# Kernel tuning notes

Hardware: AMD Instinct MI355X
Metric: run time of the kernel (lower is better)

Reference implementation:

```python
import jax, jax.numpy as jnp
import numpy as np

B, H, W, C = 4, 48, 48, 768
L = H * W
D_STATE, D_CONV, D_INNER = 16, 4, C  # expand=1
DT_RANK = (C + 15) // 16  # 48


def generate_cross_scan_indices(Hh, Ww):
    indices = []
    visited = set()
    ch, cw = Hh // 2, Ww // 2
    indices.append((ch, cw)); visited.add((ch, cw))
    for radius in range(1, max(Hh, Ww)):
        for r in range(1, radius + 1):
            p = (ch - r, cw)
            if 0 <= p[0] < Hh and 0 <= p[1] < Ww and p not in visited: indices.append(p); visited.add(p)
        for r in range(1, radius + 1):
            p = (ch, cw + r)
            if 0 <= p[0] < Hh and 0 <= p[1] < Ww and p not in visited: indices.append(p); visited.add(p)
        for r in range(1, radius + 1):
            p = (ch + r, cw)
            if 0 <= p[0] < Hh and 0 <= p[1] < Ww and p not in visited: indices.append(p); visited.add(p)
        for r in range(1, radius + 1):
            p = (ch, cw - r)
            if 0 <= p[0] < Hh and 0 <= p[1] < Ww and p not in visited: indices.append(p); visited.add(p)
        for r in range(1, radius + 1):
            for p in [(ch - r, cw + r), (ch + r, cw + r), (ch + r, cw - r), (ch - r, cw - r)]:
                if 0 <= p[0] < Hh and 0 <= p[1] < Ww and p not in visited: indices.append(p); visited.add(p)
        for i in range(-radius, radius + 1):
            for j in range(-radius, radius + 1):
                p = (ch + i, cw + j)
                if 0 <= p[0] < Hh and 0 <= p[1] < Ww and p not in visited: indices.append(p); visited.add(p)
    return np.array([i * Ww + j for i, j in indices], dtype=np.int32)


def _mamba_params(key, scale=0.02):
    ks = jax.random.split(key, 6)
    return dict(
        in_w=jax.random.normal(ks[0], (2 * D_INNER, C)) * scale,
        conv_w=jax.random.normal(ks[1], (D_INNER, 1, D_CONV)) * scale,
        conv_b=jnp.zeros((D_INNER,)),
        xproj_w=jax.random.normal(ks[2], (DT_RANK + 2 * D_STATE, D_INNER)) * scale,
        dt_w=jax.random.normal(ks[3], (D_INNER, DT_RANK)) * scale,
        dt_b=jax.random.normal(ks[4], (D_INNER,)) * 0.1,
        A_log=jnp.broadcast_to(jnp.log(jnp.arange(1, D_STATE + 1, dtype=jnp.float32)), (D_INNER, D_STATE)).copy(),
        Dp=jnp.ones((D_INNER,)),
        out_w=jax.random.normal(ks[5], (C, D_INNER)) * scale,
    )


def setup_inputs() -> dict:
    key = jax.random.key(0)
    kx, kf, kb, k1, k2 = jax.random.split(key, 5)
    fp = _mamba_params(kf)
    bp = _mamba_params(kb)
    inp = {
        'x': jax.random.normal(kx, (B, L, C), dtype=jnp.float32),
        'scan_idx': jnp.asarray(generate_cross_scan_indices(H, W)),
        'norm_g': jnp.ones((C,)), 'norm_b': jnp.zeros((C,)),
        'fuse_w1': jax.random.normal(k1, (C, 2 * C)) * 0.02, 'fuse_b1': jnp.zeros((C,)),
        'fuse_w2': jax.random.normal(k2, (C, C)) * 0.02, 'fuse_b2': jnp.zeros((C,)),
    }
    for pre, p in (('f_', fp), ('b_', bp)):
        for n, v in p.items():
            inp[pre + n] = v
    return inp


def silu(v):
    return v * jax.nn.sigmoid(v)


def mamba(x, in_w, conv_w, conv_b, xproj_w, dt_w, dt_b, A_log, Dp, out_w):
    Bn, Ln, _ = x.shape
    xz = x @ in_w.T                      # [B,L,2*d_inner]
    xi, z = jnp.split(xz, 2, axis=-1)
    # causal depthwise conv1d, kernel D_CONV, left pad D_CONV-1
    xp = jnp.pad(xi, ((0, 0), (D_CONV - 1, 0), (0, 0)))
    xc = sum(conv_w[:, 0, k] * xp[:, k:k + Ln, :] for k in range(D_CONV)) + conv_b
    xc = silu(xc)                        # [B,L,d_inner]
    x_dbl = xc @ xproj_w.T
    dt, Bm, Cm = jnp.split(x_dbl, [DT_RANK, DT_RANK + D_STATE], axis=-1)
    dt = jax.nn.softplus(dt @ dt_w.T + dt_b)  # [B,L,d_inner]
    A = -jnp.exp(A_log)                  # [d_inner,d_state]

    def step(h, inps):
        dt_t, B_t, C_t, x_t = inps       # [B,d],[B,s],[B,s],[B,d]
        dA = jnp.exp(dt_t[:, :, None] * A)
        h = dA * h + (dt_t * x_t)[:, :, None] * B_t[:, None, :]
        y = jnp.einsum('bds,bs->bd', h, C_t)
        return h, y

    h0 = jnp.zeros((Bn, D_INNER, D_STATE), xc.dtype)
    xs = (dt.transpose(1, 0, 2), Bm.transpose(1, 0, 2), Cm.transpose(1, 0, 2), xc.transpose(1, 0, 2))
    _, ys = jax.lax.scan(step, h0, xs)
    y = ys.transpose(1, 0, 2) + Dp * xc
    y = y * silu(z)
    return y @ out_w.T


def reference(x, scan_idx, norm_g, norm_b, fuse_w1, fuse_b1, fuse_w2, fuse_b2,
              f_in_w, f_conv_w, f_conv_b, f_xproj_w, f_dt_w, f_dt_b, f_A_log, f_Dp, f_out_w,
              b_in_w, b_conv_w, b_conv_b, b_xproj_w, b_dt_w, b_dt_b, b_A_log, b_Dp, b_out_w):
    residual = x
    mu = x.mean(-1, keepdims=True)
    var = ((x - mu) ** 2).mean(-1, keepdims=True)
    xn = (x - mu) / jnp.sqrt(var + 1e-6) * norm_g + norm_b
    rev = jnp.argsort(scan_idx)
    xf = mamba(xn[:, scan_idx, :], f_in_w, f_conv_w, f_conv_b, f_xproj_w, f_dt_w, f_dt_b, f_A_log, f_Dp, f_out_w)[:, rev, :]
    flip = scan_idx[::-1]
    xb = mamba(xn[:, flip, :], b_in_w, b_conv_w, b_conv_b, b_xproj_w, b_dt_w, b_dt_b, b_A_log, b_Dp, b_out_w)[:, jnp.argsort(flip), :]
    fused = jnp.concatenate([xf, xb], axis=-1)
    h = jax.nn.gelu(fused @ fuse_w1.T + fuse_b1, approximate=False)
    out = h @ fuse_w2.T + fuse_b2
    return out + residual
```

## Files before the change

kernel.cpp:

```cpp
#include <hip/hip_runtime.h>
#include <hip/hip_bf16.h>
#include <cmath>

#define BB 4
#define LL 2304
#define CC 768
#define DSTATE 16
#define DINNER 768
#define DTRANK 48
#define MTOK (BB*LL)
#define NCH 48
#define LCH (LL/NCH)

#define S_XZ   14155776L
#define S_XC   7077888L
#define S_DT   7077888L
#define S_BC   294912L
#define S_YB   7077888L
#define S_AP   2359296L

typedef __bf16 bf16_t;
typedef __bf16 bf16x8 __attribute__((ext_vector_type(8)));
typedef float  f32x4  __attribute__((ext_vector_type(4)));

__device__ __forceinline__ float silu_f(float v){ return v / (1.0f + __expf(-v)); }
__device__ __forceinline__ float softplus_f(float v){
    return fmaxf(v,0.f) + __logf(1.0f + __expf(-fabsf(v)));
}

typedef __attribute__((address_space(3))) void  lds_vt;
typedef __attribute__((address_space(1))) void  gbl_vt;
__device__ __forceinline__ void async_copy16(const void* g, void* l){
    __builtin_amdgcn_global_load_lds((const gbl_vt*)g, (lds_vt*)l, 16, 0, 0);
}

__global__ __launch_bounds__(256)
void wconv_k(const float* __restrict__ a0, const float* __restrict__ a1,
             const float* __restrict__ a2, const float* __restrict__ a3,
             const float* __restrict__ a4, const float* __restrict__ a5,
             bf16_t* __restrict__ dst)
{
    const int cum[7]  = {0,1179648,2359296,3538944,4128768,4153344,4177920};
    const int dofs[6] = {0,1179648,2359296,3538944,4718592,5332992};
    const float* srcs[6] = {a0,a1,a2,a3,a4,a5};
    int idx = blockIdx.x*256 + threadIdx.x;
    if (idx >= 4177920) return;
    int seg = 0;
    while (idx >= cum[seg+1]) ++seg;
    dst[dofs[seg] + idx - cum[seg]] = (bf16_t)srcs[seg][idx - cum[seg]];
}

__global__ __launch_bounds__(256)
void transp_k(const float* __restrict__ s0, const float* __restrict__ s1,
              bf16_t* __restrict__ d0, bf16_t* __restrict__ d1)
{
    __shared__ float tile[32][33];
    const float* src = blockIdx.z ? s1 : s0;
    bf16_t* dst = blockIdx.z ? d1 : d0;
    int c0 = blockIdx.y*32, d0c = blockIdx.x*32;
    int tx = threadIdx.x & 31, ty = threadIdx.x >> 5;
#pragma unroll
    for (int r=0;r<4;++r)
        tile[ty+8*r][tx] = src[(long)(c0+ty+8*r)*768 + d0c+tx];
    __syncthreads();
#pragma unroll
    for (int r=0;r<4;++r)
        dst[(long)(d0c+ty+8*r)*768 + c0+tx] = (bf16_t)tile[tx][ty+8*r];
}

__global__ __launch_bounds__(256)
void inv_k(const int* __restrict__ sidx, int* __restrict__ rf, int* __restrict__ rb)
{
    int t = blockIdx.x*256 + threadIdx.x;
    if (t >= LL) return;
    rf[sidx[t]] = t;
    rb[sidx[LL-1-t]] = t;
}

__global__ __launch_bounds__(256)
void combo_k(const float* __restrict__ dtw, const float* __restrict__ xproj,
             bf16_t* __restrict__ dst)
{
    __shared__ float row[48];
    int n = blockIdx.x;
    if (threadIdx.x < 48) row[threadIdx.x] = dtw[n*48 + threadIdx.x];
    __syncthreads();
#pragma unroll
    for (int kk=0; kk<3; ++kk){
        int k = threadIdx.x + 256*kk;
        float s = 0.f;
#pragma unroll 8
        for (int r=0; r<48; ++r) s += row[r]*xproj[r*768 + k];
        dst[n*768 + k] = (bf16_t)s;
    }
}

__global__ __launch_bounds__(256)
void ln_k(const float* __restrict__ x, const float* __restrict__ g,
          const float* __restrict__ bta, bf16_t* __restrict__ xn)
{
    int row = blockIdx.x;
    const float* xr = x + (long)row*CC;
    int tid = threadIdx.x;
    float v[3];
#pragma unroll
    for (int r=0;r<3;++r) v[r] = xr[tid + 256*r];
    float s  = v[0]+v[1]+v[2];
    float s2 = v[0]*v[0]+v[1]*v[1]+v[2]*v[2];
    __shared__ float red[8];
    for (int o=32;o;o>>=1){ s += __shfl_down(s,o); s2 += __shfl_down(s2,o); }
    int wv = tid>>6, ln = tid&63;
    if (ln==0){ red[wv]=s; red[4+wv]=s2; }
    __syncthreads();
    if (tid==0){
        red[0] = red[0]+red[1]+red[2]+red[3];
        red[4] = red[4]+red[5]+red[6]+red[7];
    }
    __syncthreads();
    float mu  = red[0]*(1.0f/CC);
    float var = red[4]*(1.0f/CC) - mu*mu;
    float rstd = rsqrtf(var + 1e-6f);
#pragma unroll
    for (int r=0;r<3;++r){
        int c = tid + 256*r;
        xn[(long)row*CC + c] = (bf16_t)((v[r]-mu)*rstd*g[c] + bta[c]);
    }
}

#define CT 8
__global__ __launch_bounds__(256)
void conv_k(const bf16_t* __restrict__ xz, const float* __restrict__ cw0,
            const float* __restrict__ cw1, const float* __restrict__ cb0,
            const float* __restrict__ cb1, bf16_t* __restrict__ xc)
{
    int dir = blockIdx.y;
    const bf16_t* xzd = xz + (long)dir*S_XZ;
    const float* cw = dir ? cw1 : cw0;
    const float* cb = dir ? cb1 : cb0;
    bf16_t* xcd = xc + (long)dir*S_XC;
    int idx = blockIdx.x*256 + threadIdx.x;
    if (idx >= (MTOK/CT)*(DINNER/8)) return;
    int dg    = idx % (DINNER/8);
    int chunk = idx / (DINNER/8);
    int d0 = dg*8;
    long r0 = (long)chunk*CT;
    int t0 = (int)(r0 % LL);

    float4 wv[8];
#pragma unroll
    for (int u=0;u<8;++u) wv[u] = *(const float4*)&cw[(d0+u)*4];
    float bz[8];
#pragma unroll
    for (int u=0;u<8;++u) bz[u] = cb[d0+u];

    const bf16_t* src = xzd + r0*1536 + d0;
    bf16x8 win0, win1, win2;
    if (t0 >= 3){
        win0 = *(const bf16x8*)(src - 3*1536);
        win1 = *(const bf16x8*)(src - 2*1536);
        win2 = *(const bf16x8*)(src - 1*1536);
    } else {
#pragma unroll
        for (int u=0;u<8;++u){ win0[u]=(bf16_t)0.f; win1[u]=(bf16_t)0.f; win2[u]=(bf16_t)0.f; }
    }
#pragma unroll
    for (int t=0;t<CT;++t){
        bf16x8 cur = *(const bf16x8*)(src + (long)t*1536);
        bf16x8 o;
#pragma unroll
        for (int u=0;u<8;++u){
            float acc = bz[u]
                + wv[u].x*(float)win0[u] + wv[u].y*(float)win1[u]
                + wv[u].z*(float)win2[u] + wv[u].w*(float)cur[u];
            o[u] = (bf16_t)silu_f(acc);
        }
        *(bf16x8*)(xcd + (r0+t)*DINNER + d0) = o;
        win0 = win1; win1 = win2; win2 = cur;
    }
}

template<int GATHER, int SCATTER, int EPI>
__global__ __launch_bounds__(256)
void gemm4_k(const bf16_t* __restrict__ A, long a_stride, int lda,
             const bf16_t* __restrict__ W0, const bf16_t* __restrict__ W1,
             int N, int K,
             void* __restrict__ out1, long o1_stride,
             void* __restrict__ out2, long o2_stride,
             int ldc, int ccol_stride,
             const float* __restrict__ bias0, const float* __restrict__ bias1,
             const float* __restrict__ resid,
             const int* __restrict__ sidx,
             const int* __restrict__ ridx0, const int* __restrict__ ridx1)
{
    __shared__ __align__(16) bf16_t smem[2*128*64];
    bf16_t* As = smem;
    bf16_t* Bs = smem + 128*64;

    const int tid  = threadIdx.x;
    const int lane = tid & 63;
    const int w    = tid >> 6;
    const int ln16 = lane & 15;
    const int q    = lane >> 4;
    const int dir  = blockIdx.z;

    const bf16_t* Ad = A + (long)dir*a_stride;
    const bf16_t* W  = dir ? W1 : W0;
    const float* bias = dir ? bias1 : bias0;

    const int m0 = blockIdx.x*128;
    const int n0 = blockIdx.y*128;

    const int srow = lane >> 3;
    const int csrc = (lane & 7) ^ srow;
    const bf16_t* gA[4]; const bf16_t* gA1[4]; const bf16_t* gB[4];
#pragma unroll
    for (int inst=0; inst<4; ++inst){
        int row = w*32 + inst*8 + srow;
        int r = m0 + row;
        if (GATHER == 4){
            int t = r % LL; int bo = r - t;
            gA[inst]  = A + (long)(bo + ridx0[t])*lda + csrc*8;
            gA1[inst] = A + a_stride + (long)(bo + ridx1[t])*lda + csrc*8;
        } else {
            int sr = r;
            if (GATHER == 3){
                int t = r % LL; int bo = r - t;
                sr = bo + (dir ? sidx[LL-1-t] : sidx[t]);
            }
            gA[inst] = Ad + (long)sr*lda + csrc*8;
        }
        int n = n0 + row; if (n >= N) n = N-1;
        gB[inst] = W + (long)n*K + csrc*8;
    }

    f32x4 acc[4][4];
#pragma unroll
    for (int i=0;i<4;++i)
#pragma unroll
      for (int j=0;j<4;++j) acc[i][j] = (f32x4){0.f,0.f,0.f,0.f};

    const int e = ln16 & 7;
    const int ar_base = ((w>>1)*64 + ln16)*64;
    const int br_base = ((w&1)*64 + ln16)*64;

    for (int k0 = 0; k0 < K; k0 += 64){
#pragma unroll
        for (int inst=0; inst<4; ++inst){
            bf16_t* la = As + (w*256 + inst*64)*8;
            bf16_t* lb = Bs + (w*256 + inst*64)*8;
            const bf16_t* asrc;
            if (GATHER == 4)
                asrc = (k0 >= 768) ? (gA1[inst] + (k0 - 768)) : (gA[inst] + k0);
            else
                asrc = gA[inst] + k0;
            async_copy16(asrc, la);
            async_copy16(gB[inst] + k0, lb);
        }
        __syncthreads();
#pragma unroll
        for (int kk=0; kk<2; ++kk){
            const int ce = (((kk<<2)|q) ^ e)*8;
            bf16x8 af[4], bf[4];
#pragma unroll
            for (int i=0;i<4;++i) af[i] = *(const bf16x8*)&As[ar_base + i*16*64 + ce];
#pragma unroll
            for (int j=0;j<4;++j) bf[j] = *(const bf16x8*)&Bs[br_base + j*16*64 + ce];
#pragma unroll
            for (int i=0;i<4;++i)
#pragma unroll
              for (int j=0;j<4;++j)
                acc[i][j] = __builtin_amdgcn_mfma_f32_16x16x32_bf16(af[i], bf[j], acc[i][j], 0,0,0);
        }
        __syncthreads();
    }

    const int mw = (w>>1)*64;
    const int nw = (w&1)*64;
    const int ccolb = ccol_stride*dir;

    const bool staged = (EPI==2) || (EPI==3) || (EPI==5 && n0 < 768);
    if (staged){
        bf16_t* Cs = smem;
#pragma unroll
        for (int i=0;i<4;++i){
#pragma unroll
            for (int reg=0; reg<4; ++reg){
                int rowl = mw + i*16 + q*4 + reg;
#pragma unroll
                for (int j=0;j<4;++j){
                    int coll = nw + j*16 + ln16;
                    float v = acc[i][j][reg];
                    if (EPI==3){
                        v += bias[n0 + coll];
                        v = 0.5f*v*(1.0f + erff(v*0.70710678118654752f));
                    } else if (EPI==5){
                        v = softplus_f(v + bias[n0 + coll]);
                    }
                    Cs[rowl*128 + coll] = (bf16_t)v;
                }
            }
        }
        __syncthreads();
        bf16_t* o = (bf16_t*)out1 + (long)dir*o1_stride;
#pragma unroll
        for (int c=0;c<8;++c){
            int chunk = tid + 256*c;
            int rowl = chunk >> 4;
            int coll = (chunk & 15)*8;
            int r = m0 + rowl;
            int orow = r;
            if (SCATTER == 3){
                int t = r % LL; int bo = r - t;
                orow = bo + (dir ? sidx[LL-1-t] : sidx[t]);
            }
            *(int4*)&o[(long)orow*ldc + ccolb + n0 + coll] = *(const int4*)&Cs[rowl*128 + coll];
        }
    } else {
#pragma unroll
        for (int i=0;i<4;++i){
#pragma unroll
            for (int reg=0; reg<4; ++reg){
                int r = m0 + mw + i*16 + q*4 + reg;
#pragma unroll
                for (int j=0;j<4;++j){
                    int col = n0 + nw + j*16 + ln16;
                    if (col >= N) continue;
                    float v = acc[i][j][reg];
                    if (EPI==4){
                        v += bias[col] + resid[(long)r*CC + col];
                        ((float*)out1)[(long)r*ldc + col] = v;
                    } else {
                        ((float*)out2 + (long)dir*o2_stride)[(long)r*32 + (col-768)] = v;
                    }
                }
            }
        }
    }
}

template<int PASS>
__global__ __launch_bounds__(256)
void scanp_k(const bf16_t* __restrict__ dtp, const bf16_t* __restrict__ xcp,
             const float* __restrict__ bcp, const bf16_t* __restrict__ xzp,
             const float* __restrict__ Al0, const float* __restrict__ Al1,
             const float* __restrict__ Dp0, const float* __restrict__ Dp1,
             float* __restrict__ Aprod, float* __restrict__ Hend,
             bf16_t* __restrict__ yout)
{
    extern __shared__ __align__(16) char smem[];
    bf16_t* s_dt = (bf16_t*)smem;
    bf16_t* s_xc = (bf16_t*)(smem + 6144);
    float*  s_bc = (float*) (smem + 12288);
    bf16_t* s_z  = (bf16_t*)(smem + 18432);
    bf16_t* s_y  = (bf16_t*)(smem + 24576);

    int dir = blockIdx.y;
    int blk = blockIdx.x;
    int dblk = blk % 12; int tmp = blk / 12;
    int j = tmp % NCH; int b = tmp / NCH;
    int tid = threadIdx.x;
    long tbase = (long)b*LL + (long)j*LCH;

    const bf16_t* gdt = dtp + dir*S_DT + tbase*DINNER + dblk*64;
    const bf16_t* gxc = xcp + dir*S_XC + tbase*DINNER + dblk*64;
    const float*  gbc = bcp + dir*S_BC + tbase*32;
    {
        int c = tid, t = c>>3, dc = c&7;
        async_copy16(gdt + (long)t*DINNER + dc*8, s_dt + c*8);
        async_copy16(gxc + (long)t*DINNER + dc*8, s_xc + c*8);
        async_copy16(gbc + (long)t*32 + dc*4, s_bc + c*4);
        if (tid < 128){
            c = tid + 256; t = c>>3; dc = c&7;
            async_copy16(gdt + (long)t*DINNER + dc*8, s_dt + c*8);
            async_copy16(gxc + (long)t*DINNER + dc*8, s_xc + c*8);
            async_copy16(gbc + (long)t*32 + dc*4, s_bc + c*4);
        }
    }
    if (PASS==3){
        const bf16_t* gz = xzp + dir*S_XZ + tbase*1536 + DINNER + dblk*64;
        int c = tid, t = c>>3, dc = c&7;
        async_copy16(gz + (long)t*1536 + dc*8, s_z + c*8);
        if (tid < 128){ c = tid+256; t = c>>3; dc = c&7;
            async_copy16(gz + (long)t*1536 + dc*8, s_z + c*8); }
    }
    __syncthreads();

    int lane = tid & 63, w = tid >> 6;
    int d_low = lane & 15, sg = lane >> 4;
    int dl = w*16 + d_low;
    int d  = dblk*64 + dl;

    const float* Al = dir ? Al1 : Al0;
    f32x4 al = *(const f32x4*)&Al[d*DSTATE + sg*4];
    float a_c[4];
#pragma unroll
    for (int k=0;k<4;++k) a_c[k] = -__expf(al[k]);

    float h[4] = {0.f,0.f,0.f,0.f};
    float dpv = 0.f;
    long o = dir*S_AP + ((long)(b*NCH + j)*DINNER + d)*DSTATE + sg*4;
    if (PASS==3){
        f32x4 hin = *(const f32x4*)&Aprod[o];
#pragma unroll
        for (int k=0;k<4;++k) h[k] = hin[k];
        dpv = (dir ? Dp1 : Dp0)[d];
    }
    float sdt = 0.f;

    for (int t=0; t<LCH; ++t){
        float dt = (float)s_dt[t*64 + dl];
        float xv = (float)s_xc[t*64 + dl];
        f32x4 Bv = *(const f32x4*)&s_bc[t*32 + sg*4];
        float c = dt*xv;
        if (PASS==1) sdt += dt;
#pragma unroll
        for (int k=0;k<4;++k){
            float da = __expf(dt * a_c[k]);
            h[k] = da*h[k] + c*Bv[k];
        }
        if (PASS==3){
            f32x4 Cv = *(const f32x4*)&s_bc[t*32 + 16 + sg*4];
            float p = h[0]*Cv[0] + h[1]*Cv[1] + h[2]*Cv[2] + h[3]*Cv[3];
            p += __shfl_xor(p, 16);
            p += __shfl_xor(p, 32);
            if (sg == 0){
                float z = (float)s_z[t*64 + dl];
                s_y[t*64 + dl] = (bf16_t)((p + dpv*xv) * silu_f(z));
            }
        }
    }

    if (PASS==1){
        f32x4 ap, hv;
#pragma unroll
        for (int k=0;k<4;++k){ ap[k] = __expf(sdt * a_c[k]); hv[k] = h[k]; }
        *(f32x4*)&Aprod[o] = ap;
        *(f32x4*)&Hend[o]  = hv;
    }
    if (PASS==3){
        __syncthreads();
        bf16_t* gy = yout + dir*S_YB + tbase*DINNER + dblk*64;
        int c = tid, t = c>>3, dc = c&7;
        *(int4*)(gy + (long)t*DINNER + dc*8) = *(const int4*)&s_y[c*8];
        if (tid < 128){ c = tid+256; t = c>>3; dc = c&7;
            *(int4*)(gy + (long)t*DINNER + dc*8) = *(const int4*)&s_y[c*8]; }
    }
}

__global__ __launch_bounds__(256)
void scan2_k(float* __restrict__ Aprod, const float* __restrict__ Hend)
{
    int idx = blockIdx.x*256 + threadIdx.x;
    if (idx >= 2*BB*DINNER*DSTATE) return;
    int dir = idx / (BB*DINNER*DSTATE);
    int rem = idx - dir*(BB*DINNER*DSTATE);
    int b = rem / (DINNER*DSTATE);
    int ds = rem % (DINNER*DSTATE);
    long base = (long)dir*S_AP;
    float h = 0.f;
    for (int j=0;j<NCH;++j){
        long o = base + (long)(b*NCH+j)*DINNER*DSTATE + ds;
        float ap = Aprod[o];
        float he = Hend[o];
        Aprod[o] = h;
        h = ap*h + he;
    }
}

extern "C" void kernel_launch(void* const* d_in, const int* in_sizes, int n_in,
                              void* d_out, int out_size, void* d_ws, size_t ws_size,
                              hipStream_t stream)
{
    const float* x       = (const float*)d_in[0];
    const int*   sidx    = (const int*)  d_in[1];
    const float* norm_g  = (const float*)d_in[2];
    const float* norm_b  = (const float*)d_in[3];
    const float* fuse_w1 = (const float*)d_in[4];
    const float* fuse_b1 = (const float*)d_in[5];
    const float* fuse_w2 = (const float*)d_in[6];
    const float* fuse_b2 = (const float*)d_in[7];
    const float* f_in_w   = (const float*)d_in[8];
    const float* f_conv_w = (const float*)d_in[9];
    const float* f_conv_b = (const float*)d_in[10];
    const float* f_xproj  = (const float*)d_in[11];
    const float* f_dt_w   = (const float*)d_in[12];
    const float* f_dt_b   = (const float*)d_in[13];
    const float* f_A_log  = (const float*)d_in[14];
    const float* f_Dp     = (const float*)d_in[15];
    const float* f_out_w  = (const float*)d_in[16];
    const float* b_in_w   = (const float*)d_in[17];
    const float* b_conv_w = (const float*)d_in[18];
    const float* b_conv_b = (const float*)d_in[19];
    const float* b_xproj  = (const float*)d_in[20];
    const float* b_dt_w   = (const float*)d_in[21];
    const float* b_dt_b   = (const float*)d_in[22];
    const float* b_A_log  = (const float*)d_in[23];
    const float* b_Dp     = (const float*)d_in[24];
    const float* b_out_w  = (const float*)d_in[25];
    float* out = (float*)d_out;

    float* ws    = (float*)d_ws;
    bf16_t* xn   = (bf16_t*)ws;
    bf16_t* xz   = (bf16_t*)(ws + 3538944);
    bf16_t* xc   = (bf16_t*)(ws + 17694720);
    bf16_t* dtb  = (bf16_t*)(ws + 24772608);
    float* bc    = ws + 31850496;
    bf16_t* yb   = (bf16_t*)(ws + 32440320);
    bf16_t* h1   = (bf16_t*)(ws + 39518208);
    float* Aprod = ws + 43057152;
    float* Hend  = ws + 47775744;
    bf16_t* wbf  = (bf16_t*)(ws + 52494336);
    int* rev_f   = (int*)(ws + 56352768);
    int* rev_b   = rev_f + 2304;

    bf16_t* w_fin    = wbf + 0;
    bf16_t* w_bin    = wbf + 1179648;
    bf16_t* w_1      = wbf + 2359296;
    bf16_t* w_2      = wbf + 3538944;
    bf16_t* w_fcombo = wbf + 4128768;
    bf16_t* w_bcombo = wbf + 4743168;
    bf16_t* foutT    = wbf + 5357568;
    bf16_t* boutT    = wbf + 5947392;
    bf16_t* Ccat     = wbf + 6537216;

    wconv_k<<<16320, 256, 0, stream>>>(f_in_w, b_in_w, fuse_w1, fuse_w2,
                                       f_xproj + 48*768, b_xproj + 48*768, wbf);
    transp_k<<<dim3(24,24,2), 256, 0, stream>>>(f_out_w, b_out_w, foutT, boutT);
    inv_k<<<9, 256, 0, stream>>>(sidx, rev_f, rev_b);
    combo_k<<<768, 256, 0, stream>>>(f_dt_w, f_xproj, w_fcombo);
    combo_k<<<768, 256, 0, stream>>>(b_dt_w, b_xproj, w_bcombo);
    ln_k<<<MTOK, 256, 0, stream>>>(x, norm_g, norm_b, xn);
    gemm4_k<0,0,2><<<dim3(6,6,2), 256, 0, stream>>>(
        w_1, 768, 1536, foutT, boutT, 768, 768,
        Ccat, 0, nullptr, 0, 1536, 768, nullptr, nullptr, nullptr, nullptr,
        nullptr, nullptr);

    const unsigned lds1 = 18432, lds3 = 30720;

    gemm4_k<3,0,2><<<dim3(72,12,2), 256, 0, stream>>>(
        xn, 0, CC, w_fin, w_bin, 1536, 768,
        xz, S_XZ, nullptr, 0, 1536, 0, nullptr, nullptr, nullptr, sidx,
        nullptr, nullptr);
    conv_k<<<dim3((MTOK/CT)*(DINNER/8)/256, 2), 256, 0, stream>>>(
        xz, f_conv_w, b_conv_w, f_conv_b, b_conv_b, xc);
    gemm4_k<0,0,5><<<dim3(72,7,2), 256, 0, stream>>>(
        xc, S_XC, DINNER, w_fcombo, w_bcombo, 800, 768,
        dtb, S_DT, bc, S_BC, 768, 0, f_dt_b, b_dt_b, nullptr, nullptr,
        nullptr, nullptr);
    scanp_k<1><<<dim3(BB*NCH*12,2), 256, lds1, stream>>>(
        dtb, xc, bc, nullptr, f_A_log, b_A_log, f_Dp, b_Dp, Aprod, Hend, nullptr);
    scan2_k<<<384, 256, 0, stream>>>(Aprod, Hend);
    scanp_k<3><<<dim3(BB*NCH*12,2), 256, lds3, stream>>>(
        dtb, xc, bc, xz, f_A_log, b_A_log, f_Dp, b_Dp, Aprod, Hend, yb);
    gemm4_k<4,0,3><<<dim3(72,6,1), 256, 0, stream>>>(
        yb, S_YB, DINNER, Ccat, Ccat, 768, 1536,
        h1, 0, nullptr, 0, 768, 0, fuse_b1, fuse_b1, nullptr, nullptr,
        rev_f, rev_b);
    gemm4_k<0,0,4><<<dim3(72,6,1), 256, 0, stream>>>(
        h1, 0, DINNER, w_2, w_2, 768, 768,
        out, 0, nullptr, 0, 768, 0, fuse_b2, fuse_b2, x, nullptr,
        nullptr, nullptr);
}
```

Before: 522.2 us.

## Restructure chunked scan to one channel per thread with exp-power recurrence

The chunked selective-scan kernels now give each thread one channel and all 16 states, replacing the old 4-state split and its cross-lane shuffle reductions. dt, x and z are read straight from global memory, with only B/C staged in LDS, and each block covers 256 channels, so the grid shrinks fourfold. When A_log matches log(1..16), a runtime-checked fast path computes exp(-k*dt) as powers of a single exp2, which removes 15 of 16 transcendentals per step. The cost is more registers per thread, lower occupancy, uncoalesced-looking strided global loads for dt/x/z, and a fast path that only pays off for the standard A initialisation.

```diff
diff --git a/kernel.cpp b/kernel.cpp
--- a/kernel.cpp
+++ b/kernel.cpp
@@ -18,6 +18,8 @@
 #define S_BC   294912L
 #define S_YB   7077888L
 #define S_AP   2359296L
+
+#define L2E 1.4426950408889634f
 
 typedef __bf16 bf16_t;
 typedef __bf16 bf16x8 __attribute__((ext_vector_type(8)));
@@ -347,103 +349,115 @@
              float* __restrict__ Aprod, float* __restrict__ Hend,
              bf16_t* __restrict__ yout)
 {
-    extern __shared__ __align__(16) char smem[];
-    bf16_t* s_dt = (bf16_t*)smem;
-    bf16_t* s_xc = (bf16_t*)(smem + 6144);
-    float*  s_bc = (float*) (smem + 12288);
-    bf16_t* s_z  = (bf16_t*)(smem + 18432);
-    bf16_t* s_y  = (bf16_t*)(smem + 24576);
-
-    int dir = blockIdx.y;
+    __shared__ __align__(16) float s_bc[LCH*32];
+
+    const int dir = blockIdx.y;
     int blk = blockIdx.x;
-    int dblk = blk % 12; int tmp = blk / 12;
-    int j = tmp % NCH; int b = tmp / NCH;
-    int tid = threadIdx.x;
-    long tbase = (long)b*LL + (long)j*LCH;
-
-    const bf16_t* gdt = dtp + dir*S_DT + tbase*DINNER + dblk*64;
-    const bf16_t* gxc = xcp + dir*S_XC + tbase*DINNER + dblk*64;
-    const float*  gbc = bcp + dir*S_BC + tbase*32;
-    {
-        int c = tid, t = c>>3, dc = c&7;
-        async_copy16(gdt + (long)t*DINNER + dc*8, s_dt + c*8);
-        async_copy16(gxc + (long)t*DINNER + dc*8, s_xc + c*8);
-        async_copy16(gbc + (long)t*32 + dc*4, s_bc + c*4);
-        if (tid < 128){
-            c = tid + 256; t = c>>3; dc = c&7;
-            async_copy16(gdt + (long)t*DINNER + dc*8, s_dt + c*8);
-            async_copy16(gxc + (long)t*DINNER + dc*8, s_xc + c*8);
-            async_copy16(gbc + (long)t*32 + dc*4, s_bc + c*4);
-        }
-    }
+    const int dblk = blk % 3; int tmp = blk / 3;
+    const int j = tmp % NCH; const int b = tmp / NCH;
+    const int tid = threadIdx.x;
+    const long tbase = (long)b*LL + (long)j*LCH;
+    const int d = dblk*256 + tid;
+
+    const float* gbc = bcp + dir*S_BC + tbase*32;
+    async_copy16(gbc + tid*4, s_bc + tid*4);
+    if (tid < 128) async_copy16(gbc + (256+tid)*4, s_bc + (256+tid)*4);
+
+    const float* Al = dir ? Al1 : Al0;
+    float ac2[16]; bool fast = true;
+#pragma unroll
+    for (int k=0;k<16;++k){
+        float a = -__expf(Al[d*DSTATE + k]);
+        fast = fast && (fabsf(a + (float)(k+1)) < 1e-3f*(float)(k+1));
+        ac2[k] = a * L2E;
+    }
+
+    __syncthreads();
+
+    const bf16_t* gdt = dtp + dir*S_DT + tbase*DINNER + d;
+    const bf16_t* gxc = xcp + dir*S_XC + tbase*DINNER + d;
+    const bf16_t* gz  = xzp + dir*S_XZ + tbase*1536 + DINNER + d;
+    bf16_t* gy = yout + dir*S_YB + tbase*DINNER + d;
+
+    const long o = dir*S_AP + ((long)(b*NCH + j)*DINNER + d)*DSTATE;
+
+    float h[16];
+    float dpv = 0.f;
     if (PASS==3){
-        const bf16_t* gz = xzp + dir*S_XZ + tbase*1536 + DINNER + dblk*64;
-        int c = tid, t = c>>3, dc = c&7;
-        async_copy16(gz + (long)t*1536 + dc*8, s_z + c*8);
-        if (tid < 128){ c = tid+256; t = c>>3; dc = c&7;
-            async_copy16(gz + (long)t*1536 + dc*8, s_z + c*8); }
-    }
-    __syncthreads();
-
-    int lane = tid & 63, w = tid >> 6;
-    int d_low = lane & 15, sg = lane >> 4;
-    int dl = w*16 + d_low;
-    int d  = dblk*64 + dl;
-
-    const float* Al = dir ? Al1 : Al0;
-    f32x4 al = *(const f32x4*)&Al[d*DSTATE + sg*4];
-    float a_c[4];
-#pragma unroll
-    for (int k=0;k<4;++k) a_c[k] = -__expf(al[k]);
-
-    float h[4] = {0.f,0.f,0.f,0.f};
-    float dpv = 0.f;
-    long o = dir*S_AP + ((long)(b*NCH + j)*DINNER + d)*DSTATE + sg*4;
-    if (PASS==3){
-        f32x4 hin = *(const f32x4*)&Aprod[o];
-#pragma unroll
-        for (int k=0;k<4;++k) h[k] = hin[k];
+#pragma unroll
+        for (int g=0; g<4; ++g){
+            f32x4 hv = *(const f32x4*)&Aprod[o + 4*g];
+#pragma unroll
+            for (int k=0;k<4;++k) h[g*4+k] = hv[k];
+        }
         dpv = (dir ? Dp1 : Dp0)[d];
+    } else {
+#pragma unroll
+        for (int k=0;k<16;++k) h[k] = 0.f;
     }
     float sdt = 0.f;
 
+#pragma unroll 2
     for (int t=0; t<LCH; ++t){
-        float dt = (float)s_dt[t*64 + dl];
-        float xv = (float)s_xc[t*64 + dl];
-        f32x4 Bv = *(const f32x4*)&s_bc[t*32 + sg*4];
+        float dt = (float)gdt[(long)t*DINNER];
+        float xv = (float)gxc[(long)t*DINNER];
+        float ek[16];
+        if (fast){
+            float e1 = __builtin_amdgcn_exp2f(-L2E*dt);
+            ek[0]=e1;        ek[1]=e1*e1;      ek[2]=ek[1]*e1;   ek[3]=ek[1]*ek[1];
+            ek[4]=ek[3]*e1;  ek[5]=ek[3]*ek[1];ek[6]=ek[3]*ek[2];ek[7]=ek[3]*ek[3];
+            ek[8]=ek[7]*e1;  ek[9]=ek[7]*ek[1];ek[10]=ek[7]*ek[2];ek[11]=ek[7]*ek[3];
+            ek[12]=ek[7]*ek[4];ek[13]=ek[7]*ek[5];ek[14]=ek[7]*ek[6];ek[15]=ek[7]*ek[7];
+        } else {
+#pragma unroll
+            for (int k=0;k<16;++k) ek[k] = __builtin_amdgcn_exp2f(dt*ac2[k]);
+        }
         float c = dt*xv;
         if (PASS==1) sdt += dt;
-#pragma unroll
-        for (int k=0;k<4;++k){
-            float da = __expf(dt * a_c[k]);
-            h[k] = da*h[k] + c*Bv[k];
+        const float* bcr = &s_bc[t*32];
+#pragma unroll
+        for (int g=0; g<4; ++g){
+            f32x4 Bv = *(const f32x4*)&bcr[g*4];
+#pragma unroll
+            for (int k=0;k<4;++k) h[g*4+k] = ek[g*4+k]*h[g*4+k] + c*Bv[k];
         }
         if (PASS==3){
-            f32x4 Cv = *(const f32x4*)&s_bc[t*32 + 16 + sg*4];
-            float p = h[0]*Cv[0] + h[1]*Cv[1] + h[2]*Cv[2] + h[3]*Cv[3];
-            p += __shfl_xor(p, 16);
-            p += __shfl_xor(p, 32);
-            if (sg == 0){
-                float z = (float)s_z[t*64 + dl];
-                s_y[t*64 + dl] = (bf16_t)((p + dpv*xv) * silu_f(z));
+            f32x4 Cv0 = *(const f32x4*)&bcr[16];
+            f32x4 Cv1 = *(const f32x4*)&bcr[20];
+            f32x4 Cv2 = *(const f32x4*)&bcr[24];
+            f32x4 Cv3 = *(const f32x4*)&bcr[28];
+            float p0=0.f,p1=0.f,p2=0.f,p3=0.f;
+#pragma unroll
+            for (int k=0;k<4;++k){
+                p0 += h[k]*Cv0[k];    p1 += h[4+k]*Cv1[k];
+                p2 += h[8+k]*Cv2[k];  p3 += h[12+k]*Cv3[k];
             }
+            float p = (p0+p1)+(p2+p3);
+            float zv = (float)gz[(long)t*1536];
+            gy[(long)t*DINNER] = (bf16_t)((p + dpv*xv) * silu_f(zv));
         }
     }
 
     if (PASS==1){
-        f32x4 ap, hv;
-#pragma unroll
-        for (int k=0;k<4;++k){ ap[k] = __expf(sdt * a_c[k]); hv[k] = h[k]; }
-        *(f32x4*)&Aprod[o] = ap;
-        *(f32x4*)&Hend[o]  = hv;
-    }
-    if (PASS==3){
-        __syncthreads();
-        bf16_t* gy = yout + dir*S_YB + tbase*DINNER + dblk*64;
-        int c = tid, t = c>>3, dc = c&7;
-        *(int4*)(gy + (long)t*DINNER + dc*8) = *(const int4*)&s_y[c*8];
-        if (tid < 128){ c = tid+256; t = c>>3; dc = c&7;
-            *(int4*)(gy + (long)t*DINNER + dc*8) = *(const int4*)&s_y[c*8]; }
+        float ap[16];
+        if (fast){
+            float e1 = __builtin_amdgcn_exp2f(-L2E*sdt);
+            ap[0]=e1;        ap[1]=e1*e1;      ap[2]=ap[1]*e1;   ap[3]=ap[1]*ap[1];
+            ap[4]=ap[3]*e1;  ap[5]=ap[3]*ap[1];ap[6]=ap[3]*ap[2];ap[7]=ap[3]*ap[3];
+            ap[8]=ap[7]*e1;  ap[9]=ap[7]*ap[1];ap[10]=ap[7]*ap[2];ap[11]=ap[7]*ap[3];
+            ap[12]=ap[7]*ap[4];ap[13]=ap[7]*ap[5];ap[14]=ap[7]*ap[6];ap[15]=ap[7]*ap[7];
+        } else {
+#pragma unroll
+            for (int k=0;k<16;++k) ap[k] = __builtin_amdgcn_exp2f(sdt*ac2[k]);
+        }
+#pragma unroll
+        for (int g=0; g<4; ++g){
+            f32x4 av, hv;
+#pragma unroll
+            for (int k=0;k<4;++k){ av[k]=ap[g*4+k]; hv[k]=h[g*4+k]; }
+            *(f32x4*)&Aprod[o+4*g] = av;
+            *(f32x4*)&Hend[o+4*g]  = hv;
+        }
     }
 }
 
@@ -535,8 +549,6 @@
         Ccat, 0, nullptr, 0, 1536, 768, nullptr, nullptr, nullptr, nullptr,
         nullptr, nullptr);
 
-    const unsigned lds1 = 18432, lds3 = 30720;
-
     gemm4_k<3,0,2><<<dim3(72,12,2), 256, 0, stream>>>(
         xn, 0, CC, w_fin, w_bin, 1536, 768,
         xz, S_XZ, nullptr, 0, 1536, 0, nullptr, nullptr, nullptr, sidx,
@@ -547,10 +559,10 @@
         xc, S_XC, DINNER, w_fcombo, w_bcombo, 800, 768,
         dtb, S_DT, bc, S_BC, 768, 0, f_dt_b, b_dt_b, nullptr, nullptr,
         nullptr, nullptr);
-    scanp_k<1><<<dim3(BB*NCH*12,2), 256, lds1, stream>>>(
-        dtb, xc, bc, nullptr, f_A_log, b_A_log, f_Dp, b_Dp, Aprod, Hend, nullptr);
+    scanp_k<1><<<dim3(BB*NCH*3,2), 256, 0, stream>>>(
+        dtb, xc, bc, xz, f_A_log, b_A_log, f_Dp, b_Dp, Aprod, Hend, yb);
     scan2_k<<<384, 256, 0, stream>>>(Aprod, Hend);
-    scanp_k<3><<<dim3(BB*NCH*12,2), 256, lds3, stream>>>(
+    scanp_k<3><<<dim3(BB*NCH*3,2), 256, 0, stream>>>(
         dtb, xc, bc, xz, f_A_log, b_A_log, f_Dp, b_Dp, Aprod, Hend, yb);
     gemm4_k<4,0,3><<<dim3(72,6,1), 256, 0, stream>>>(
         yb, S_YB, DINNER, Ccat, Ccat, 768, 1536,
```

Result: faster. 505.8 us (-3.1%).
